# Performance work log

Measured on AMD Instinct MI355X. Metric: run time of the kernel, lower is better.

## Reference

```python
import jax, jax.numpy as jnp
import numpy as np

N_NODES = 100000


def gcn_conv(x, edge_index, W, b, add_self_loops=True):
    """PyG GCNConv: out = D^{-1/2}(A+I)D^{-1/2} (x @ W) + b, sum-aggregated at col."""
    n = x.shape[0]
    x = x @ W  # linear first, like PyG (smaller feature dim usually)
    row, col = edge_index[0], edge_index[1]
    if add_self_loops:
        loop = jnp.arange(n, dtype=row.dtype)
        row = jnp.concatenate([row, loop])
        col = jnp.concatenate([col, loop])
    ones = jnp.ones(row.shape[0], dtype=x.dtype)
    deg = jax.ops.segment_sum(ones, col, num_segments=n)  # in-degree incl. self loops
    dinv = jnp.where(deg > 0, jax.lax.rsqrt(deg), 0.0)
    norm = dinv[row] * dinv[col]  # [E]
    msg = x[row] * norm[:, None]  # gather + scale, [E, F]
    out = jax.ops.segment_sum(msg, col, num_segments=n)  # scatter-add
    return out + b


def setup_inputs() -> dict:
    key = jax.random.key(0)
    ks = jax.random.split(key, 12)
    latent_dim, condition_dim, hidden_dim, output_dim = 64, 32, 64, 64
    n_edges = 1600000
    latent = jax.random.normal(ks[0], (N_NODES, latent_dim), dtype=jnp.float32)
    condition = jax.random.normal(ks[1], (N_NODES, condition_dim), dtype=jnp.float32)
    edge_index = jax.random.randint(ks[2], (2, n_edges), 0, N_NODES, dtype=jnp.int64 if jax.config.jax_enable_x64 else jnp.int32)

    def glorot(k, fan_in, fan_out):
        s = jnp.sqrt(6.0 / (fan_in + fan_out))
        return jax.random.uniform(k, (fan_in, fan_out), minval=-s, maxval=s, dtype=jnp.float32)

    W1 = glorot(ks[3], latent_dim, hidden_dim); b1 = jnp.zeros((hidden_dim,), jnp.float32)
    W2 = glorot(ks[4], condition_dim, hidden_dim); b2 = jnp.zeros((hidden_dim,), jnp.float32)
    W3 = glorot(ks[5], 2 * hidden_dim, hidden_dim); b3 = jnp.zeros((hidden_dim,), jnp.float32)
    W4 = glorot(ks[6], hidden_dim, output_dim); b4 = jnp.zeros((output_dim,), jnp.float32)
    return {"latent": latent, "condition": condition, "edge_index": edge_index,
            "W1": W1, "b1": b1, "W2": W2, "b2": b2,
            "W3": W3, "b3": b3, "W4": W4, "b4": b4}


def reference(latent, condition, edge_index, W1, b1, W2, b2, W3, b3, W4, b4):
    z2h = gcn_conv(latent, edge_index, W1, b1)
    c2h = gcn_conv(condition, edge_index, W2, b2)
    h = jnp.concatenate([z2h, c2h], axis=1)
    h = gcn_conv(h, edge_index, W3, b3)
    out = gcn_conv(h, edge_index, W4, b4)
    return out
```

## Files before the change

kernel.cpp:

```cpp
#include <hip/hip_runtime.h>
#include <hip/hip_fp16.h>

#define BKN 4
#define CBN 256
#define CHUNK 4096
#define MAXBIN 5120

typedef _Float16 half8 __attribute__((ext_vector_type(8)));
typedef _Float16 h4v __attribute__((ext_vector_type(4)));
typedef float floatx4 __attribute__((ext_vector_type(4)));


__global__ void init_cur_kernel(int* __restrict__ p, int n, int stride) {
    int i = blockIdx.x * blockDim.x + threadIdx.x;
    if (i < n) p[i] = i * stride;
}


__global__ __launch_bounds__(256) void passA_kernel(const int* __restrict__ ei,
                                                    int* __restrict__ curCB,
                                                    unsigned* __restrict__ binned,
                                                    int E, int NCB) {
    __shared__ int lcnt[512];
    __shared__ int sA[512], sB[512];
    __shared__ int loffx[512];
    __shared__ int gbase[512];
    __shared__ int lpos[512];
    __shared__ unsigned stage[CHUNK];
    __shared__ unsigned short sbin[CHUNK];
    int tid = threadIdx.x;
    int base = blockIdx.x * CHUNK;
    for (int i = tid; i < 512; i += 256) lcnt[i] = 0;
    __syncthreads();
    unsigned pk[16]; int bin[16];
    #pragma unroll
    for (int q = 0; q < 16; ++q) {
        int e = base + q * 256 + tid;
        if (e < E) {
            int r = ei[e], c = ei[E + e];
            pk[q] = ((unsigned)r << 8) | (unsigned)(c & 255);
            bin[q] = c >> 8;
            atomicAdd(&lcnt[bin[q]], 1);
        } else bin[q] = -1;
    }
    __syncthreads();
    for (int i = tid; i < 512; i += 256) sA[i] = lcnt[i];
    __syncthreads();
    int* src = sA; int* dst = sB;
    for (int o = 1; o < 512; o <<= 1) {
        for (int i = tid; i < 512; i += 256)
            dst[i] = src[i] + (i >= o ? src[i - o] : 0);
        __syncthreads();
        int* t = src; src = dst; dst = t;
    }
    for (int i = tid; i < 512; i += 256) {
        int ex = (i > 0) ? src[i - 1] : 0;
        loffx[i] = ex;
        lpos[i] = ex;
        int c = lcnt[i];
        gbase[i] = (c > 0 && i < NCB) ? atomicAdd(&curCB[i], c) : 0;
    }
    __syncthreads();
    #pragma unroll
    for (int q = 0; q < 16; ++q) {
        if (bin[q] >= 0) {
            int p = atomicAdd(&lpos[bin[q]], 1);
            stage[p] = pk[q];
            sbin[p] = (unsigned short)bin[q];
        }
    }
    __syncthreads();
    int total = min(CHUNK, E - base);
    for (int idx = tid; idx < total; idx += 256) {
        int b2 = sbin[idx];
        binned[gbase[b2] + (idx - loffx[b2])] = stage[idx];
    }
}


__global__ __launch_bounds__(256) void passB_kernel(const unsigned* __restrict__ binned,
                                                    const int* __restrict__ curCB,
                                                    unsigned* __restrict__ bkt,
                                                    int* __restrict__ offB,
                                                    int* __restrict__ offE,
                                                    float* __restrict__ dinv,
                                                    int N, int NCB, int NB) {
    __shared__ unsigned raw[MAXBIN];
    __shared__ unsigned stage[MAXBIN];
    __shared__ int fcnt[64], foff[65], fpos[64];
    __shared__ int ncnt[256];
    int i = blockIdx.x;
    int tid = threadIdx.x;
    int g0 = i * MAXBIN;
    int cnt = curCB[i] - g0;
    if (cnt > MAXBIN) cnt = MAXBIN;
    for (int j = tid; j < 64; j += 256) fcnt[j] = 0;
    ncnt[tid] = 0;
    __syncthreads();
    for (int idx = tid; idx < cnt; idx += 256) {
        unsigned pk = binned[g0 + idx];
        raw[idx] = pk;
        atomicAdd(&fcnt[(pk >> 2) & 63], 1);
        atomicAdd(&ncnt[pk & 255], 1);
    }
    __syncthreads();
    if (tid == 0) {
        int run = 0;
        for (int j = 0; j < 64; ++j) { foff[j] = run; run += fcnt[j]; }
        foff[64] = run;
    }
    __syncthreads();
    if (tid < 64) fpos[tid] = foff[tid];
    __syncthreads();
    for (int idx = tid; idx < cnt; idx += 256) {
        unsigned pk = raw[idx];
        int p = atomicAdd(&fpos[(pk >> 2) & 63], 1);
        stage[p] = ((pk >> 8) << 2) | (pk & 3);
    }
    __syncthreads();
    for (int idx = tid; idx < cnt; idx += 256) bkt[g0 + idx] = stage[idx];
    int fb0 = i * 64;
    int nfb = min(64, NB - fb0);
    for (int j = tid; j < nfb; j += 256) {
        offB[fb0 + j] = g0 + foff[j];
        offE[fb0 + j] = g0 + foff[j + 1];
    }
    int n0 = i * CBN;
    int n = n0 + tid;
    if (n < N) dinv[n] = rsqrtf((float)ncnt[tid] + 1.0f);
}

__global__ __launch_bounds__(256) void fold_kernel(
    const float* __restrict__ W1, const float* __restrict__ b1,
    const float* __restrict__ W2, const float* __restrict__ b2,
    const float* __restrict__ W3, const float* __restrict__ b3,
    const float* __restrict__ W4,
    float* __restrict__ Wf1, float* __restrict__ Wf2,
    float* __restrict__ u, float* __restrict__ v) {
    __shared__ float As[64][64];
    __shared__ float gsl[64];
    int tid = threadIdx.x;
    int f = tid & 63;
    int w = __builtin_amdgcn_readfirstlane(tid >> 6);
    int blk = blockIdx.x;

    float w4c[64];
    #pragma unroll
    for (int k = 0; k < 64; ++k) w4c[k] = W4[k * 64 + f];

    if (blk < 24) {
        const int half = (blk < 16) ? 0 : 64;
        #pragma unroll 2
        for (int kk = 0; kk < 16; ++kk) {
            int k = w * 16 + kk;
            float a = 0.f;
            #pragma unroll
            for (int j = 0; j < 64; ++j)
                a += W3[(half + k) * 64 + j] * w4c[j];
            As[k][f] = a;
        }
        __syncthreads();
        const float* Wsrc = (blk < 16) ? W1 : W2;
        float* Wdst = (blk < 16) ? Wf1 : Wf2;
        int i = ((blk < 16) ? blk : (blk - 16)) * 4 + w;
        float a = 0.f;
        #pragma unroll
        for (int k = 0; k < 64; ++k)
            a += Wsrc[i * 64 + k] * As[k][f];
        Wdst[i * 64 + f] = a;
    } else {
        float g = 0.f;
        #pragma unroll
        for (int k = 0; k < 64; ++k) g += b1[k] * W3[k * 64 + f];
        #pragma unroll
        for (int k = 0; k < 64; ++k) g += b2[k] * W3[(64 + k) * 64 + f];
        if (w == 0) gsl[f] = g;
        __syncthreads();
        if (w == 0) {
            float uu = 0.f, vv = 0.f;
            #pragma unroll
            for (int k = 0; k < 64; ++k) {
                uu += gsl[k] * w4c[k];
                vv += b3[k] * w4c[k];
            }
            u[f] = uu;
            v[f] = vv;
        }
    }
}

__global__ __launch_bounds__(256) void linZ_kernel(
    const float* __restrict__ lat, const float* __restrict__ cond,
    const float* __restrict__ Wf1, const float* __restrict__ Wf2,
    const float* __restrict__ dinv, _Float16* __restrict__ Z, int N) {
    __shared__ _Float16 Xs[64][104];
    __shared__ _Float16 Wt[64][104];
    int tid = threadIdx.x;
    int n0 = blockIdx.x * 64;
    {
        const float4* lat4 = (const float4*)(lat + (size_t)n0 * 64);
        #pragma unroll
        for (int q = 0; q < 4; ++q) {
            int idx = q * 256 + tid;
            int row = idx >> 4;
            float4 v = make_float4(0.f, 0.f, 0.f, 0.f);
            if (n0 + row < N) v = lat4[idx];
            int col = (idx & 15) * 4;
            Xs[row][col + 0] = (_Float16)v.x;
            Xs[row][col + 1] = (_Float16)v.y;
            Xs[row][col + 2] = (_Float16)v.z;
            Xs[row][col + 3] = (_Float16)v.w;
        }
        const float4* cond4 = (const float4*)(cond + (size_t)n0 * 32);
        #pragma unroll
        for (int q = 0; q < 2; ++q) {
            int idx = q * 256 + tid;
            int row = idx >> 3;
            float4 v = make_float4(0.f, 0.f, 0.f, 0.f);
            if (n0 + row < N) v = cond4[idx];
            int col = 64 + (idx & 7) * 4;
            Xs[row][col + 0] = (_Float16)v.x;
            Xs[row][col + 1] = (_Float16)v.y;
            Xs[row][col + 2] = (_Float16)v.z;
            Xs[row][col + 3] = (_Float16)v.w;
        }
        for (int i = tid; i < 4096; i += 256) {
            int k = i >> 6, f = i & 63;
            Wt[f][k] = (_Float16)Wf1[i];
        }
        for (int i = tid; i < 2048; i += 256) {
            int k = i >> 6, f = i & 63;
            Wt[f][64 + k] = (_Float16)Wf2[i];
        }
    }
    __syncthreads();
    int lane = tid & 63, wave = tid >> 6;
    int quad = lane >> 4, l16 = lane & 15;
    floatx4 acc[4] = {};
    #pragma unroll
    for (int kc = 0; kc < 96; kc += 32) {
        half8 a = *(const half8*)&Xs[wave * 16 + l16][kc + quad * 8];
        #pragma unroll
        for (int nt = 0; nt < 4; ++nt) {
            half8 b = *(const half8*)&Wt[nt * 16 + l16][kc + quad * 8];
            acc[nt] = __builtin_amdgcn_mfma_f32_16x16x32_f16(a, b, acc[nt], 0, 0, 0);
        }
    }
    #pragma unroll
    for (int r = 0; r < 4; ++r) {
        int n = n0 + wave * 16 + quad * 4 + r;
        if (n < N) {
            float d = dinv[n];
            #pragma unroll
            for (int nt = 0; nt < 4; ++nt)
                Z[(size_t)n * 64 + nt * 16 + l16] = (_Float16)(acc[nt][r] * d);
        }
    }
}

template <bool FINAL>
__global__ __launch_bounds__(256) void hop_kernel(
    const _Float16* __restrict__ Vp, const float* __restrict__ dinv,
    const int* __restrict__ offB, const int* __restrict__ offE,
    const unsigned* __restrict__ bkt,
    const float* __restrict__ wvec, void* __restrict__ outv, int NB) {
    int lane = threadIdx.x & 63;
    int wave = threadIdx.x >> 6;
    int b = blockIdx.x * 4 + wave;
    if (b >= NB) return;
    int g  = lane >> 4;
    int fq = lane & 15;
    int c0 = b * BKN;

    float acc[4][4];
    {
        h4v h = *(const h4v*)&Vp[(size_t)(c0 + g) * 64 + fq * 4];
        #pragma unroll
        for (int t = 0; t < 4; ++t)
            #pragma unroll
            for (int j = 0; j < 4; ++j)
                acc[t][j] = (t == g) ? (float)h[j] : 0.f;
    }

    int s = offB[b], e = offE[b];
    #pragma unroll 4
    for (int i0 = s; i0 < e; i0 += 4) {
        int idx = i0 + g;
        unsigned pk = bkt[min(idx, e - 1)];
        int te = (idx < e) ? (int)(pk & 3u) : 4;
        int r  = (int)(pk >> 2);
        h4v h = *(const h4v*)&Vp[(size_t)r * 64 + fq * 4];
        float v0 = (float)h[0], v1 = (float)h[1];
        float v2 = (float)h[2], v3 = (float)h[3];
        #pragma unroll
        for (int t = 0; t < 4; ++t) {
            float sel = (te == t) ? 1.f : 0.f;
            acc[t][0] = fmaf(sel, v0, acc[t][0]);
            acc[t][1] = fmaf(sel, v1, acc[t][1]);
            acc[t][2] = fmaf(sel, v2, acc[t][2]);
            acc[t][3] = fmaf(sel, v3, acc[t][3]);
        }
    }

    #pragma unroll
    for (int t = 0; t < 4; ++t)
        #pragma unroll
        for (int j = 0; j < 4; ++j) {
            float x = acc[t][j];
            x += __shfl_xor(x, 16, 64);
            x += __shfl_xor(x, 32, 64);
            acc[t][j] = x;
        }

    float og[4];
    #pragma unroll
    for (int j = 0; j < 4; ++j) {
        float x0 = (g == 0) ? acc[0][j] : acc[1][j];
        float x1 = (g == 2) ? acc[2][j] : acc[3][j];
        og[j] = (g < 2) ? x0 : x1;
    }
    float d = dinv[c0 + g];
    float4 wv = *(const float4*)&wvec[fq * 4];
    if constexpr (FINAL) {
        float4 o;
        o.x = og[0] * d + wv.x;
        o.y = og[1] * d + wv.y;
        o.z = og[2] * d + wv.z;
        o.w = og[3] * d + wv.w;
        *(float4*)&((float*)outv)[(size_t)(c0 + g) * 64 + fq * 4] = o;
    } else {
        float dd = d * d;
        h4v o;
        o[0] = (_Float16)(og[0] * dd + d * wv.x);
        o[1] = (_Float16)(og[1] * dd + d * wv.y);
        o[2] = (_Float16)(og[2] * dd + d * wv.z);
        o[3] = (_Float16)(og[3] * dd + d * wv.w);
        *(h4v*)&((_Float16*)outv)[(size_t)(c0 + g) * 64 + fq * 4] = o;
    }
}


static inline size_t align256(size_t x) { return (x + 255) & ~(size_t)255; }

extern "C" void kernel_launch(void* const* d_in, const int* in_sizes, int n_in,
                              void* d_out, int out_size, void* d_ws, size_t ws_size,
                              hipStream_t stream) {
    const float* latent = (const float*)d_in[0];
    const float* cond   = (const float*)d_in[1];
    const int*   ei     = (const int*)d_in[2];
    const float* W1 = (const float*)d_in[3];
    const float* b1 = (const float*)d_in[4];
    const float* W2 = (const float*)d_in[5];
    const float* b2 = (const float*)d_in[6];
    const float* W3 = (const float*)d_in[7];
    const float* b3 = (const float*)d_in[8];
    const float* W4 = (const float*)d_in[9];
    const float* b4 = (const float*)d_in[10];
    float* out = (float*)d_out;

    const int N = in_sizes[0] / 64;
    const int E = in_sizes[2] / 2;
    const int NB  = (N + BKN - 1) / BKN;
    const int NCB = (N + CBN - 1) / CBN;
    const int NCH = (E + CHUNK - 1) / CHUNK;
    const size_t REG = (size_t)NCB * MAXBIN;

    char* w = (char*)d_ws;
    size_t o = 0;
    int* curCB = (int*)(w + o); o = align256(o + (size_t)NCB * 4);
    int* offB  = (int*)(w + o); o = align256(o + (size_t)NB * 4);
    int* offE  = (int*)(w + o); o = align256(o + (size_t)NB * 4);
    float* dinv = (float*)(w + o); o = align256(o + (size_t)N * 4);
    float* Wf1 = (float*)(w + o); o = align256(o + 4096 * 4);
    float* Wf2 = (float*)(w + o); o = align256(o + 2048 * 4);
    float* uVec = (float*)(w + o); o = align256(o + 64 * 4);
    float* vVec = (float*)(w + o); o = align256(o + 64 * 4);
    unsigned* binned = (unsigned*)(w + o); o = align256(o + REG * 4);
    unsigned* bkt    = (unsigned*)(w + o); o = align256(o + REG * 4);
    _Float16* Z = (_Float16*)(w + o); o = align256(o + (size_t)N * 64 * 2);
    _Float16* P = (_Float16*)(w + o); o = align256(o + (size_t)N * 64 * 2);

    const int BS = 256;
    int gHop = (NB + 3) / 4;

    init_cur_kernel<<<2, BS, 0, stream>>>(curCB, NCB, MAXBIN);
    passA_kernel<<<NCH, BS, 0, stream>>>(ei, curCB, binned, E, NCB);
    passB_kernel<<<NCB, BS, 0, stream>>>(binned, curCB, bkt, offB, offE, dinv, N, NCB, NB);

    fold_kernel<<<25, BS, 0, stream>>>(W1, b1, W2, b2, W3, b3, W4, Wf1, Wf2, uVec, vVec);
    linZ_kernel<<<(N + 63) / 64, BS, 0, stream>>>(latent, cond, Wf1, Wf2, dinv, Z, N);

    hop_kernel<false><<<gHop, BS, 0, stream>>>(Z, dinv, offB, offE, bkt, uVec, (void*)P, NB);
    hop_kernel<false><<<gHop, BS, 0, stream>>>(P, dinv, offB, offE, bkt, vVec, (void*)Z, NB);
    hop_kernel<true ><<<gHop, BS, 0, stream>>>(Z, dinv, offB, offE, bkt, b4, (void*)out, NB);
}
```

Baseline: 259.2 us.

## Switch to per-node CSR and feature-sliced Z layout for hop gathers

PassB now builds a per-node CSR (offsets, ends, row ids) using a parallel scan instead of 4-node buckets with packed target bits. The intermediate feature matrices are stored in four 16-feature slices of 32 bytes per node, and each hop block handles one slice, so the gathered working set per slice is smaller and more likely to stay in cache. Each 4-lane group owns one destination node and accumulates directly, with no select-FMA masking and no cross-lane shuffle reduction. The cost is four times more blocks, each re-reading the index lists, and load imbalance from per-node degree variation.

```diff
diff --git a/kernel.cpp b/kernel.cpp
--- a/kernel.cpp
+++ b/kernel.cpp
@@ -80,54 +80,53 @@
 
 __global__ __launch_bounds__(256) void passB_kernel(const unsigned* __restrict__ binned,
                                                     const int* __restrict__ curCB,
-                                                    unsigned* __restrict__ bkt,
-                                                    int* __restrict__ offB,
-                                                    int* __restrict__ offE,
+                                                    int* __restrict__ bktR,
+                                                    int* __restrict__ offN,
+                                                    int* __restrict__ endN,
                                                     float* __restrict__ dinv,
-                                                    int N, int NCB, int NB) {
+                                                    int N, int NCB) {
     __shared__ unsigned raw[MAXBIN];
-    __shared__ unsigned stage[MAXBIN];
-    __shared__ int fcnt[64], foff[65], fpos[64];
-    __shared__ int ncnt[256];
+    __shared__ int stageR[MAXBIN];
+    __shared__ int fcnt[256], foff[256], fpos[256];
+    __shared__ int sA[256], sB[256];
     int i = blockIdx.x;
     int tid = threadIdx.x;
     int g0 = i * MAXBIN;
     int cnt = curCB[i] - g0;
     if (cnt > MAXBIN) cnt = MAXBIN;
-    for (int j = tid; j < 64; j += 256) fcnt[j] = 0;
-    ncnt[tid] = 0;
+    fcnt[tid] = 0;
     __syncthreads();
     for (int idx = tid; idx < cnt; idx += 256) {
         unsigned pk = binned[g0 + idx];
         raw[idx] = pk;
-        atomicAdd(&fcnt[(pk >> 2) & 63], 1);
-        atomicAdd(&ncnt[pk & 255], 1);
-    }
-    __syncthreads();
-    if (tid == 0) {
-        int run = 0;
-        for (int j = 0; j < 64; ++j) { foff[j] = run; run += fcnt[j]; }
-        foff[64] = run;
-    }
-    __syncthreads();
-    if (tid < 64) fpos[tid] = foff[tid];
+        atomicAdd(&fcnt[pk & 255], 1);
+    }
+    __syncthreads();
+    sA[tid] = fcnt[tid];
+    __syncthreads();
+    int* src = sA; int* dst = sB;
+    for (int o = 1; o < 256; o <<= 1) {
+        dst[tid] = src[tid] + (tid >= o ? src[tid - o] : 0);
+        __syncthreads();
+        int* t = src; src = dst; dst = t;
+    }
+    int excl = src[tid] - fcnt[tid];
+    foff[tid] = excl;
+    fpos[tid] = excl;
     __syncthreads();
     for (int idx = tid; idx < cnt; idx += 256) {
         unsigned pk = raw[idx];
-        int p = atomicAdd(&fpos[(pk >> 2) & 63], 1);
-        stage[p] = ((pk >> 8) << 2) | (pk & 3);
-    }
-    __syncthreads();
-    for (int idx = tid; idx < cnt; idx += 256) bkt[g0 + idx] = stage[idx];
-    int fb0 = i * 64;
-    int nfb = min(64, NB - fb0);
-    for (int j = tid; j < nfb; j += 256) {
-        offB[fb0 + j] = g0 + foff[j];
-        offE[fb0 + j] = g0 + foff[j + 1];
-    }
-    int n0 = i * CBN;
-    int n = n0 + tid;
-    if (n < N) dinv[n] = rsqrtf((float)ncnt[tid] + 1.0f);
+        int p = atomicAdd(&fpos[pk & 255], 1);
+        stageR[p] = (int)(pk >> 8);
+    }
+    __syncthreads();
+    for (int idx = tid; idx < cnt; idx += 256) bktR[g0 + idx] = stageR[idx];
+    int n = i * CBN + tid;
+    if (n < N) {
+        offN[n] = g0 + foff[tid];
+        endN[n] = g0 + foff[tid] + fcnt[tid];
+        dinv[n] = rsqrtf((float)fcnt[tid] + 1.0f);
+    }
 }
 
 __global__ __launch_bounds__(256) void fold_kernel(
@@ -253,7 +252,7 @@
             float d = dinv[n];
             #pragma unroll
             for (int nt = 0; nt < 4; ++nt)
-                Z[(size_t)n * 64 + nt * 16 + l16] = (_Float16)(acc[nt][r] * d);
+                Z[(size_t)nt * N * 16 + (size_t)n * 16 + l16] = (_Float16)(acc[nt][r] * d);
         }
     }
 }
@@ -261,81 +260,65 @@
 template <bool FINAL>
 __global__ __launch_bounds__(256) void hop_kernel(
     const _Float16* __restrict__ Vp, const float* __restrict__ dinv,
-    const int* __restrict__ offB, const int* __restrict__ offE,
-    const unsigned* __restrict__ bkt,
-    const float* __restrict__ wvec, void* __restrict__ outv, int NB) {
+    const int* __restrict__ offN, const int* __restrict__ endN,
+    const int* __restrict__ bktR,
+    const float* __restrict__ wvec, void* __restrict__ outv,
+    int N, int WPS) {
+    int bid = blockIdx.x;
+    int sl  = bid / WPS;
+    int wg  = bid % WPS;
     int lane = threadIdx.x & 63;
     int wave = threadIdx.x >> 6;
-    int b = blockIdx.x * 4 + wave;
-    if (b >= NB) return;
-    int g  = lane >> 4;
-    int fq = lane & 15;
-    int c0 = b * BKN;
-
-    float acc[4][4];
+    int nl = lane >> 2;
+    int fl = lane & 3;
+    int n = wg * 64 + wave * 16 + nl;
+    if (n >= N) return;
+    const _Float16* Vs = Vp + (size_t)sl * N * 16;
+
+    float a0, a1, a2, a3;
     {
-        h4v h = *(const h4v*)&Vp[(size_t)(c0 + g) * 64 + fq * 4];
-        #pragma unroll
-        for (int t = 0; t < 4; ++t)
-            #pragma unroll
-            for (int j = 0; j < 4; ++j)
-                acc[t][j] = (t == g) ? (float)h[j] : 0.f;
-    }
-
-    int s = offB[b], e = offE[b];
-    #pragma unroll 4
-    for (int i0 = s; i0 < e; i0 += 4) {
-        int idx = i0 + g;
-        unsigned pk = bkt[min(idx, e - 1)];
-        int te = (idx < e) ? (int)(pk & 3u) : 4;
-        int r  = (int)(pk >> 2);
-        h4v h = *(const h4v*)&Vp[(size_t)r * 64 + fq * 4];
-        float v0 = (float)h[0], v1 = (float)h[1];
-        float v2 = (float)h[2], v3 = (float)h[3];
-        #pragma unroll
-        for (int t = 0; t < 4; ++t) {
-            float sel = (te == t) ? 1.f : 0.f;
-            acc[t][0] = fmaf(sel, v0, acc[t][0]);
-            acc[t][1] = fmaf(sel, v1, acc[t][1]);
-            acc[t][2] = fmaf(sel, v2, acc[t][2]);
-            acc[t][3] = fmaf(sel, v3, acc[t][3]);
-        }
-    }
-
-    #pragma unroll
-    for (int t = 0; t < 4; ++t)
-        #pragma unroll
-        for (int j = 0; j < 4; ++j) {
-            float x = acc[t][j];
-            x += __shfl_xor(x, 16, 64);
-            x += __shfl_xor(x, 32, 64);
-            acc[t][j] = x;
-        }
-
-    float og[4];
-    #pragma unroll
-    for (int j = 0; j < 4; ++j) {
-        float x0 = (g == 0) ? acc[0][j] : acc[1][j];
-        float x1 = (g == 2) ? acc[2][j] : acc[3][j];
-        og[j] = (g < 2) ? x0 : x1;
-    }
-    float d = dinv[c0 + g];
-    float4 wv = *(const float4*)&wvec[fq * 4];
+        h4v h = *(const h4v*)&Vs[(size_t)n * 16 + fl * 4];
+        a0 = (float)h[0]; a1 = (float)h[1]; a2 = (float)h[2]; a3 = (float)h[3];
+    }
+    int s = offN[n], e = endN[n];
+    int idx = s;
+    for (; idx + 4 <= e; idx += 4) {
+        int r0 = bktR[idx + 0];
+        int r1 = bktR[idx + 1];
+        int r2 = bktR[idx + 2];
+        int r3 = bktR[idx + 3];
+        h4v h0 = *(const h4v*)&Vs[(size_t)r0 * 16 + fl * 4];
+        h4v h1 = *(const h4v*)&Vs[(size_t)r1 * 16 + fl * 4];
+        h4v h2 = *(const h4v*)&Vs[(size_t)r2 * 16 + fl * 4];
+        h4v h3 = *(const h4v*)&Vs[(size_t)r3 * 16 + fl * 4];
+        a0 += (float)h0[0] + (float)h1[0] + (float)h2[0] + (float)h3[0];
+        a1 += (float)h0[1] + (float)h1[1] + (float)h2[1] + (float)h3[1];
+        a2 += (float)h0[2] + (float)h1[2] + (float)h2[2] + (float)h3[2];
+        a3 += (float)h0[3] + (float)h1[3] + (float)h2[3] + (float)h3[3];
+    }
+    for (; idx < e; ++idx) {
+        int r = bktR[idx];
+        h4v h = *(const h4v*)&Vs[(size_t)r * 16 + fl * 4];
+        a0 += (float)h[0]; a1 += (float)h[1]; a2 += (float)h[2]; a3 += (float)h[3];
+    }
+
+    float d = dinv[n];
+    float4 wv = *(const float4*)&wvec[sl * 16 + fl * 4];
     if constexpr (FINAL) {
         float4 o;
-        o.x = og[0] * d + wv.x;
-        o.y = og[1] * d + wv.y;
-        o.z = og[2] * d + wv.z;
-        o.w = og[3] * d + wv.w;
-        *(float4*)&((float*)outv)[(size_t)(c0 + g) * 64 + fq * 4] = o;
+        o.x = a0 * d + wv.x;
+        o.y = a1 * d + wv.y;
+        o.z = a2 * d + wv.z;
+        o.w = a3 * d + wv.w;
+        *(float4*)&((float*)outv)[(size_t)n * 64 + sl * 16 + fl * 4] = o;
     } else {
         float dd = d * d;
         h4v o;
-        o[0] = (_Float16)(og[0] * dd + d * wv.x);
-        o[1] = (_Float16)(og[1] * dd + d * wv.y);
-        o[2] = (_Float16)(og[2] * dd + d * wv.z);
-        o[3] = (_Float16)(og[3] * dd + d * wv.w);
-        *(h4v*)&((_Float16*)outv)[(size_t)(c0 + g) * 64 + fq * 4] = o;
+        o[0] = (_Float16)(a0 * dd + d * wv.x);
+        o[1] = (_Float16)(a1 * dd + d * wv.y);
+        o[2] = (_Float16)(a2 * dd + d * wv.z);
+        o[3] = (_Float16)(a3 * dd + d * wv.w);
+        *(h4v*)&((_Float16*)outv)[(size_t)sl * N * 16 + (size_t)n * 16 + fl * 4] = o;
     }
 }
 
@@ -360,7 +343,6 @@
 
     const int N = in_sizes[0] / 64;
     const int E = in_sizes[2] / 2;
-    const int NB  = (N + BKN - 1) / BKN;
     const int NCB = (N + CBN - 1) / CBN;
     const int NCH = (E + CHUNK - 1) / CHUNK;
     const size_t REG = (size_t)NCB * MAXBIN;
@@ -368,29 +350,30 @@
     char* w = (char*)d_ws;
     size_t o = 0;
     int* curCB = (int*)(w + o); o = align256(o + (size_t)NCB * 4);
-    int* offB  = (int*)(w + o); o = align256(o + (size_t)NB * 4);
-    int* offE  = (int*)(w + o); o = align256(o + (size_t)NB * 4);
+    int* offN  = (int*)(w + o); o = align256(o + (size_t)N * 4);
+    int* endN  = (int*)(w + o); o = align256(o + (size_t)N * 4);
     float* dinv = (float*)(w + o); o = align256(o + (size_t)N * 4);
     float* Wf1 = (float*)(w + o); o = align256(o + 4096 * 4);
     float* Wf2 = (float*)(w + o); o = align256(o + 2048 * 4);
     float* uVec = (float*)(w + o); o = align256(o + 64 * 4);
     float* vVec = (float*)(w + o); o = align256(o + 64 * 4);
     unsigned* binned = (unsigned*)(w + o); o = align256(o + REG * 4);
-    unsigned* bkt    = (unsigned*)(w + o); o = align256(o + REG * 4);
+    int* bktR        = (int*)(w + o); o = align256(o + REG * 4);
     _Float16* Z = (_Float16*)(w + o); o = align256(o + (size_t)N * 64 * 2);
     _Float16* P = (_Float16*)(w + o); o = align256(o + (size_t)N * 64 * 2);
 
     const int BS = 256;
-    int gHop = (NB + 3) / 4;
+    const int WPS = (N + 63) / 64;
+    const int gHop = 4 * WPS;
 
     init_cur_kernel<<<2, BS, 0, stream>>>(curCB, NCB, MAXBIN);
     passA_kernel<<<NCH, BS, 0, stream>>>(ei, curCB, binned, E, NCB);
-    passB_kernel<<<NCB, BS, 0, stream>>>(binned, curCB, bkt, offB, offE, dinv, N, NCB, NB);
+    passB_kernel<<<NCB, BS, 0, stream>>>(binned, curCB, bktR, offN, endN, dinv, N, NCB);
 
     fold_kernel<<<25, BS, 0, stream>>>(W1, b1, W2, b2, W3, b3, W4, Wf1, Wf2, uVec, vVec);
     linZ_kernel<<<(N + 63) / 64, BS, 0, stream>>>(latent, cond, Wf1, Wf2, dinv, Z, N);
 
-    hop_kernel<false><<<gHop, BS, 0, stream>>>(Z, dinv, offB, offE, bkt, uVec, (void*)P, NB);
-    hop_kernel<false><<<gHop, BS, 0, stream>>>(P, dinv, offB, offE, bkt, vVec, (void*)Z, NB);
-    hop_kernel<true ><<<gHop, BS, 0, stream>>>(Z, dinv, offB, offE, bkt, b4, (void*)out, NB);
-}
+    hop_kernel<false><<<gHop, BS, 0, stream>>>(Z, dinv, offN, endN, bktR, uVec, (void*)P, N, WPS);
+    hop_kernel<false><<<gHop, BS, 0, stream>>>(P, dinv, offN, endN, bktR, vVec, (void*)Z, N, WPS);
+    hop_kernel<true ><<<gHop, BS, 0, stream>>>(Z, dinv, offN, endN, bktR, b4, (void*)out, N, WPS);
+}
```

Result: slower. 325.4 us (+25.5%).
